# Kernel tuning notes

Hardware: AMD Instinct MI355X
Metric: run time of the kernel (lower is better)

The kernel has to match this reference:

```python
import jax, jax.numpy as jnp
import numpy as np

B, SQ, SKV, D = 4, 4096, 4096, 64

def setup_inputs() -> dict:
    key = jax.random.key(0)
    kq, kv = jax.random.split(key)
    query = jax.random.normal(kq, (B, SQ, D), dtype=jnp.float32)
    value = jax.random.normal(kv, (B, SKV, D), dtype=jnp.float32)
    return {"query": query, "value": value}

def reference(query, value):
    # scores = Q @ V^T  (value acts as both keys and values; no 1/sqrt(d) scaling)
    scores = jnp.einsum('bqd,bkd->bqk', query, value)  # [B, SQ, SKV]
    dist = jax.nn.softmax(scores, axis=-1)
    context = jnp.einsum('bqk,bkd->bqd', dist, value)  # [B, SQ, D]
    return context
```

## Files before the change

### kernel.cpp

```cpp
#include <hip/hip_runtime.h>
#include <type_traits>


#define NB   4
#define SQ   4096
#define SKV  4096
#define DH   64
#define L2E  1.44269504088896340736f

typedef _Float16 half8 __attribute__((ext_vector_type(8)));
typedef _Float16 half4 __attribute__((ext_vector_type(4)));
typedef _Float16 half2v __attribute__((ext_vector_type(2)));
typedef float f32x4 __attribute__((ext_vector_type(4)));
typedef unsigned short u16;

#define MFMA16(a, b, c) __builtin_amdgcn_mfma_f32_16x16x16f16((a), (b), (c), 0, 0, 0)
#define MFMA32(a, b, c) __builtin_amdgcn_mfma_f32_16x16x32_f16((a), (b), (c), 0, 0, 0)

__device__ __forceinline__ u16 f2h(float f) {
  _Float16 h = (_Float16)f;
  return __builtin_bit_cast(u16, h);
}
__device__ __forceinline__ half2v pkrtz(float a, float b) {
  return __builtin_bit_cast(half2v, __builtin_amdgcn_cvt_pkrtz(a, b));
}
__device__ __forceinline__ float fmax3(float a, float b, float c) {
  return fmaxf(fmaxf(a, b), c);
}

typedef __attribute__((address_space(1))) void gvoid;
typedef __attribute__((address_space(3))) void lvoid;
__device__ __forceinline__ void dma16(const u16* g, u16* l) {
  __builtin_amdgcn_global_load_lds((gvoid*)g, (lvoid*)l, 16, 0, 0);
}

__global__ __launch_bounds__(256) void prep_kernel(
    const float* __restrict__ V, u16* __restrict__ vh, u16* __restrict__ vt) {
  __shared__ u16 ldsT[16 * 72];
  int blk = blockIdx.x;
  int x   = blk & 7;
  int b   = x >> 1;
  int rem = ((x & 1) << 7) + (blk >> 3);
  int j0  = (rem >> 2) << 6;
  int d0  = (rem & 3) << 4;
  int t   = threadIdx.x;
  int j   = t >> 2;
  int dc  = (t & 3) << 2;

  const float* src = V + ((size_t)(b * SKV) + j0 + j) * DH + d0 + dc;
  float4 v4 = *(const float4*)src;
  u16 h[4] = {f2h(v4.x), f2h(v4.y), f2h(v4.z), f2h(v4.w)};
  unsigned p0 = (unsigned)h[0] | ((unsigned)h[1] << 16);
  unsigned p1 = (unsigned)h[2] | ((unsigned)h[3] << 16);
  int dfull = d0 + dc;
  int physd = ((((dfull >> 3) ^ (j & 7)) << 3)) + (dfull & 7);
  *(uint2*)(vh + ((size_t)(b * SKV) + j0 + j) * DH + physd) = make_uint2(p0, p1);

#pragma unroll
  for (int k = 0; k < 4; ++k) ldsT[(dc + k) * 72 + j] = h[k];
  __syncthreads();

  int dl = t >> 4;
  int jc = (t & 15) << 2;
  u16 tr[4];
#pragma unroll
  for (int k = 0; k < 4; ++k) tr[k] = ldsT[dl * 72 + jc + k];
  unsigned q0 = (unsigned)tr[0] | ((unsigned)tr[1] << 16);
  unsigned q1 = (unsigned)tr[2] | ((unsigned)tr[3] << 16);
  int d   = d0 + dl;
  int kc2 = jc >> 5;
  int g   = (jc >> 4) & 1;
  int qd  = (jc >> 2) & 3;
  int hp  = ((kc2 << 2) | qd) ^ (d & 7);
  *(uint2*)(vt + ((size_t)(b * DH) + d) * SKV + j0 + (hp << 3) + (g << 2)) =
      make_uint2(q0, q1);
}

__global__ __launch_bounds__(256, 4) void attn_kernel(
    const float* __restrict__ Q,
    const u16* __restrict__ vh,
    const u16* __restrict__ vt,
    u16* __restrict__ po,
    float* __restrict__ pm,
    float* __restrict__ pl,
    int S, int kvLen) {
  __shared__ __align__(16) u16 lds[2][2][4096];

  int blk  = blockIdx.x;
  int tile, s;
  if (S == 4) {
    int x  = blk & 7;
    int jj = ((x & 1) << 7) + (blk >> 3);
    tile   = ((x >> 1) << 6) + (jj >> 2);
    s      = jj & 3;
  } else {
    tile = blk / S;
    s    = blk - tile * S;
  }
  int b    = tile >> 6;
  int q0   = (tile & 63) << 6;
  int kv0  = s * kvLen;
  int t    = threadIdx.x;
  int wave = t >> 6;
  int lane = t & 63;
  int col  = lane & 15;
  int quad = lane >> 4;
  int qw   = q0 + (wave << 4);
  int c7   = col & 7;

  const u16* gv  = vh + (size_t)(b * SKV) * DH;
  const u16* gvt = vt + (size_t)(b * DH) * SKV;

  int r0 = t >> 3;
  int c0 = (t & 7) << 3;
  int wb = wave << 9;

  half8 qf[2];
#pragma unroll
  for (int kc = 0; kc < 2; ++kc) {
    const float* qp = Q + ((size_t)(b * SQ) + qw + col) * DH + kc * 32 + (quad << 3);
    float4 a0 = *(const float4*)qp;
    float4 a1 = *(const float4*)(qp + 4);
    half8 hq;
    hq[0] = (_Float16)(a0.x * L2E); hq[1] = (_Float16)(a0.y * L2E);
    hq[2] = (_Float16)(a0.z * L2E); hq[3] = (_Float16)(a0.w * L2E);
    hq[4] = (_Float16)(a1.x * L2E); hq[5] = (_Float16)(a1.y * L2E);
    hq[6] = (_Float16)(a1.z * L2E); hq[7] = (_Float16)(a1.w * L2E);
    qf[kc] = hq;
  }

  f32x4 o[4];
#pragma unroll
  for (int nf = 0; nf < 4; ++nf) o[nf] = (f32x4){0.f, 0.f, 0.f, 0.f};
  float m_r = -1e30f, l_r = 0.f;

  half4 pf[4];
  half8 vr[8];

  int ch0 = quad ^ c7;
  int ch1 = ch0 ^ 4;
  const char* Lb = (const char*)&lds[0][0][0];
  const char* a0p = Lb + (col << 7) + (ch0 << 4);
  const char* a1p = Lb + (col << 7) + (ch1 << 4);

  const u16* pvh  = gv + ((size_t)(kv0 + r0) << 6) + c0;
  const u16* pvh2 = pvh + 2048;
  const u16* pvt  = gvt + (size_t)r0 * SKV + kv0 + c0;
  const u16* pvt2 = pvt + (size_t)32 * SKV;

  dma16(pvh,  &lds[0][0][0] + wb);
  dma16(pvh2, &lds[0][0][0] + 2048 + wb);
  dma16(pvt,  &lds[0][1][0] + wb);
  dma16(pvt2, &lds[0][1][0] + 2048 + wb);
  pvh += 4096; pvh2 += 4096; pvt += 64; pvt2 += 64;

  int nIter = kvLen >> 6;

  auto body = [&](auto BUFC, int it_) {
    constexpr int BUF = decltype(BUFC)::value;
    constexpr int BO  = BUF * 16384;
    __syncthreads();

    if (it_ + 1 < nIter) {
      dma16(pvh,  &lds[BUF ^ 1][0][0] + wb);
      dma16(pvh2, &lds[BUF ^ 1][0][0] + 2048 + wb);
      dma16(pvt,  &lds[BUF ^ 1][1][0] + wb);
      dma16(pvt2, &lds[BUF ^ 1][1][0] + 2048 + wb);
    }
    pvh += 4096; pvh2 += 4096; pvt += 64; pvt2 += 64;

    __builtin_amdgcn_s_setprio(1);
    if (it_ > 0) {
#pragma unroll
      for (int kc2 = 0; kc2 < 2; ++kc2) {
#pragma unroll
        for (int nf2 = 0; nf2 < 4; ++nf2) {
          half8 w8 = vr[kc2 * 4 + nf2];
          half4 wlo = __builtin_shufflevector(w8, w8, 0, 1, 2, 3);
          half4 whi = __builtin_shufflevector(w8, w8, 4, 5, 6, 7);
          o[nf2] = MFMA16(wlo, pf[kc2 * 2], o[nf2]);
          o[nf2] = MFMA16(whi, pf[kc2 * 2 + 1], o[nf2]);
        }
      }
    }

    f32x4 sf[4];
#pragma unroll
    for (int nf = 0; nf < 4; ++nf) sf[nf] = (f32x4){0.f, 0.f, 0.f, 0.f};
#pragma unroll
    for (int nf = 0; nf < 4; ++nf) {
      half8 av0 = *(const half8*)(a0p + BO + nf * 2048);
      sf[nf] = MFMA32(av0, qf[0], sf[nf]);
      half8 av1 = *(const half8*)(a1p + BO + nf * 2048);
      sf[nf] = MFMA32(av1, qf[1], sf[nf]);
    }
    __builtin_amdgcn_s_setprio(0);

    {
      float t0 = fmax3(sf[0][0], sf[0][1], sf[0][2]);
      float t1 = fmax3(sf[0][3], sf[1][0], sf[1][1]);
      float t2 = fmax3(sf[1][2], sf[1][3], sf[2][0]);
      float t3 = fmax3(sf[2][1], sf[2][2], sf[2][3]);
      float t4 = fmax3(sf[3][0], sf[3][1], sf[3][2]);
      float t5 = fmax3(t0, t1, sf[3][3]);
      float tm = fmax3(t2, t3, t4);
      tm = fmaxf(tm, t5);
      tm = fmaxf(tm, __shfl_xor(tm, 16, 64));
      tm = fmaxf(tm, __shfl_xor(tm, 32, 64));
      float mn = fmaxf(m_r, tm);
      float al = 1.0f;
      if (!__all(mn == m_r)) {
        al = exp2f(m_r - mn);
        m_r = mn;
#pragma unroll
        for (int nf = 0; nf < 4; ++nf)
#pragma unroll
          for (int r = 0; r < 4; ++r) o[nf][r] *= al;
      }
      float rs = 0.f;
#pragma unroll
      for (int nf = 0; nf < 4; ++nf) {
        float p0 = exp2f(sf[nf][0] - mn);
        float p1 = exp2f(sf[nf][1] - mn);
        float p2 = exp2f(sf[nf][2] - mn);
        float p3 = exp2f(sf[nf][3] - mn);
        rs += (p0 + p1) + (p2 + p3);
        half2v lo = pkrtz(p0, p1);
        half2v hi = pkrtz(p2, p3);
        pf[nf] = __builtin_shufflevector(lo, hi, 0, 1, 2, 3);
      }
      l_r = l_r * al + rs;
    }

#pragma unroll
    for (int nf2 = 0; nf2 < 4; ++nf2) {
      vr[nf2]     = *(const half8*)(a0p + BO + 8192 + nf2 * 2048);
      vr[4 + nf2] = *(const half8*)(a1p + BO + 8192 + nf2 * 2048);
    }
  };

  for (int it = 0; it < nIter; it += 2) {
    body(std::integral_constant<int, 0>{}, it);
    body(std::integral_constant<int, 1>{}, it + 1);
  }

  __builtin_amdgcn_s_setprio(1);
#pragma unroll
  for (int kc2 = 0; kc2 < 2; ++kc2) {
#pragma unroll
    for (int nf2 = 0; nf2 < 4; ++nf2) {
      half8 w8 = vr[kc2 * 4 + nf2];
      half4 wlo = __builtin_shufflevector(w8, w8, 0, 1, 2, 3);
      half4 whi = __builtin_shufflevector(w8, w8, 4, 5, 6, 7);
      o[nf2] = MFMA16(wlo, pf[kc2 * 2], o[nf2]);
      o[nf2] = MFMA16(whi, pf[kc2 * 2 + 1], o[nf2]);
    }
  }
  __builtin_amdgcn_s_setprio(0);

  l_r += __shfl_xor(l_r, 16, 64);
  l_r += __shfl_xor(l_r, 32, 64);
  int pidx = tile * S + s;
  if (quad == 0) {
    pm[(size_t)pidx * 64 + (wave << 4) + col] = m_r;
    pl[(size_t)pidx * 64 + (wave << 4) + col] = l_r;
  }

  __syncthreads();
  u16* tp = &lds[0][0][0];
  {
    int qrow = (wave << 4) + col;
#pragma unroll
    for (int nf2 = 0; nf2 < 4; ++nf2) {
#pragma unroll
      for (int r2 = 0; r2 < 4; r2 += 2) {
        unsigned pk = (unsigned)f2h(o[nf2][r2]) |
                      ((unsigned)f2h(o[nf2][r2 + 1]) << 16);
        int d = nf2 * 16 + (quad << 2) + r2;
        *(unsigned*)(tp + qrow * 72 + d) = pk;
      }
    }
  }
  __syncthreads();
  {
    u16* pob = po + (size_t)pidx * 64 * 64;
    int q = t >> 2, hc = (t & 3) << 4;
    uint4 x0 = *(const uint4*)(tp + q * 72 + hc);
    uint4 x1 = *(const uint4*)(tp + q * 72 + hc + 8);
    *(uint4*)(pob + q * 64 + hc)     = x0;
    *(uint4*)(pob + q * 64 + hc + 8) = x1;
  }
}

__global__ __launch_bounds__(256) void combine_kernel(
    const u16* __restrict__ po,
    const float* __restrict__ pm,
    const float* __restrict__ pl,
    float* __restrict__ out, int S) {
  int t    = threadIdx.x;
  int rowg;
  if (S == 4) {
    int x  = blockIdx.x & 7;
    int j2 = ((x & 1) << 6) + (blockIdx.x >> 3);
    int tile = ((x >> 1) << 6) + (j2 >> 1);
    rowg = tile * 64 + ((j2 & 1) << 5) + (t >> 3);
  } else {
    rowg = blockIdx.x * 32 + (t >> 3);
  }
  int tile = rowg >> 6;
  int row  = rowg & 63;
  int dc   = (t & 7) << 3;

  float mv[8], lv[8];
  float M = -1e30f;
#pragma unroll
  for (int s = 0; s < 8; ++s) {
    if (s < S) {
      mv[s] = pm[(size_t)(tile * S + s) * 64 + row];
      lv[s] = pl[(size_t)(tile * S + s) * 64 + row];
      M = fmaxf(M, mv[s]);
    }
  }
  float L = 0.f, w[8];
#pragma unroll
  for (int s = 0; s < 8; ++s) {
    if (s < S) {
      w[s] = exp2f(mv[s] - M);
      L += lv[s] * w[s];
    }
  }
  float acc[8] = {0.f, 0.f, 0.f, 0.f, 0.f, 0.f, 0.f, 0.f};
#pragma unroll
  for (int s = 0; s < 8; ++s) {
    if (s < S) {
      const u16* p = po + (size_t)(tile * S + s) * 4096 + row * 64 + dc;
      uint4 raw = *(const uint4*)p;
      half8 x = __builtin_bit_cast(half8, raw);
#pragma unroll
      for (int k = 0; k < 8; ++k) acc[k] += w[s] * (float)x[k];
    }
  }
  float invL = 1.0f / L;
  float* op = out + (size_t)rowg * 64 + dc;
  f32x4 o0 = (f32x4){acc[0], acc[1], acc[2], acc[3]};
  f32x4 o1 = (f32x4){acc[4], acc[5], acc[6], acc[7]};
  *(f32x4*)op       = o0 * invL;
  *(f32x4*)(op + 4) = o1 * invL;
}

extern "C" void kernel_launch(void* const* d_in, const int* in_sizes, int n_in,
                              void* d_out, int out_size, void* d_ws, size_t ws_size,
                              hipStream_t stream) {
  const float* Q = (const float*)d_in[0];
  const float* V = (const float*)d_in[1];
  float* out = (float*)d_out;

  const size_t convBytes = (size_t)2 * NB * SKV * DH * 2;
  auto partBytes = [](int S) {
    return (size_t)NB * 64 * S * ((size_t)64 * 64 * 2 + 64 * 8);
  };
  int S = 4;
  while (S > 1 && ws_size < convBytes + partBytes(S)) S >>= 1;
  int kvLen = SKV / S;

  u16* vh = (u16*)d_ws;
  u16* vt = vh + (size_t)NB * SKV * DH;
  u16* po = vt + (size_t)NB * SKV * DH;
  float* pm = (float*)(po + (size_t)NB * 64 * S * 64 * 64);
  float* pl = pm + (size_t)NB * 64 * S * 64;

  prep_kernel<<<NB * 256, 256, 0, stream>>>(V, vh, vt);
  attn_kernel<<<NB * 64 * S, 256, 0, stream>>>(Q, vh, vt, po, pm, pl, S, kvLen);
  combine_kernel<<<NB * SQ / 32, 256, 0, stream>>>(po, pm, pl, out, S);
}
```

Measured before the change: 105.5 us.

## Interleave deferred PV MFMAs with QK row-max cross-lane shuffles

Moves the deferred P·V MFMAs from the previous iteration so they run after the QK score MFMAs. Each half is placed between the two cross-lane shuffle steps of the row-max reduction, so shuffle latency overlaps with matrix work. The accumulator rescale by alpha is moved after the exp/pack loop. This lengthens live ranges of the sf/pf/vr registers and could raise register pressure or change how the scheduler orders work.

```diff
diff --git a/kernel.cpp b/kernel.cpp
--- a/kernel.cpp
+++ b/kernel.cpp
@@ -169,24 +169,10 @@
     }
     pvh += 4096; pvh2 += 4096; pvt += 64; pvt2 += 64;
 
+    f32x4 sf[4];
+#pragma unroll
+    for (int nf = 0; nf < 4; ++nf) sf[nf] = (f32x4){0.f, 0.f, 0.f, 0.f};
     __builtin_amdgcn_s_setprio(1);
-    if (it_ > 0) {
-#pragma unroll
-      for (int kc2 = 0; kc2 < 2; ++kc2) {
-#pragma unroll
-        for (int nf2 = 0; nf2 < 4; ++nf2) {
-          half8 w8 = vr[kc2 * 4 + nf2];
-          half4 wlo = __builtin_shufflevector(w8, w8, 0, 1, 2, 3);
-          half4 whi = __builtin_shufflevector(w8, w8, 4, 5, 6, 7);
-          o[nf2] = MFMA16(wlo, pf[kc2 * 2], o[nf2]);
-          o[nf2] = MFMA16(whi, pf[kc2 * 2 + 1], o[nf2]);
-        }
-      }
-    }
-
-    f32x4 sf[4];
-#pragma unroll
-    for (int nf = 0; nf < 4; ++nf) sf[nf] = (f32x4){0.f, 0.f, 0.f, 0.f};
 #pragma unroll
     for (int nf = 0; nf < 4; ++nf) {
       half8 av0 = *(const half8*)(a0p + BO + nf * 2048);
@@ -196,26 +182,53 @@
     }
     __builtin_amdgcn_s_setprio(0);
 
+    float t0 = fmax3(sf[0][0], sf[0][1], sf[0][2]);
+    float t1 = fmax3(sf[0][3], sf[1][0], sf[1][1]);
+    float t2 = fmax3(sf[1][2], sf[1][3], sf[2][0]);
+    float t3 = fmax3(sf[2][1], sf[2][2], sf[2][3]);
+    float t4 = fmax3(sf[3][0], sf[3][1], sf[3][2]);
+    float t5 = fmax3(t0, t1, sf[3][3]);
+    float tmw = fmax3(t2, t3, t4);
+    tmw = fmaxf(tmw, t5);
+    float tx = __shfl_xor(tmw, 16, 64);
+
+    if (it_ > 0) {
+      __builtin_amdgcn_s_setprio(1);
+#pragma unroll
+      for (int nf2 = 0; nf2 < 4; ++nf2) {
+        half8 w8 = vr[nf2];
+        half4 wlo = __builtin_shufflevector(w8, w8, 0, 1, 2, 3);
+        half4 whi = __builtin_shufflevector(w8, w8, 4, 5, 6, 7);
+        o[nf2] = MFMA16(wlo, pf[0], o[nf2]);
+        o[nf2] = MFMA16(whi, pf[1], o[nf2]);
+      }
+      __builtin_amdgcn_s_setprio(0);
+    }
+
+    float tm2 = fmaxf(tmw, tx);
+    float ty = __shfl_xor(tm2, 32, 64);
+
+    if (it_ > 0) {
+      __builtin_amdgcn_s_setprio(1);
+#pragma unroll
+      for (int nf2 = 0; nf2 < 4; ++nf2) {
+        half8 w8 = vr[4 + nf2];
+        half4 wlo = __builtin_shufflevector(w8, w8, 0, 1, 2, 3);
+        half4 whi = __builtin_shufflevector(w8, w8, 4, 5, 6, 7);
+        o[nf2] = MFMA16(wlo, pf[2], o[nf2]);
+        o[nf2] = MFMA16(whi, pf[3], o[nf2]);
+      }
+      __builtin_amdgcn_s_setprio(0);
+    }
+
     {
-      float t0 = fmax3(sf[0][0], sf[0][1], sf[0][2]);
-      float t1 = fmax3(sf[0][3], sf[1][0], sf[1][1]);
-      float t2 = fmax3(sf[1][2], sf[1][3], sf[2][0]);
-      float t3 = fmax3(sf[2][1], sf[2][2], sf[2][3]);
-      float t4 = fmax3(sf[3][0], sf[3][1], sf[3][2]);
-      float t5 = fmax3(t0, t1, sf[3][3]);
-      float tm = fmax3(t2, t3, t4);
-      tm = fmaxf(tm, t5);
-      tm = fmaxf(tm, __shfl_xor(tm, 16, 64));
-      tm = fmaxf(tm, __shfl_xor(tm, 32, 64));
+      float tm = fmaxf(tm2, ty);
       float mn = fmaxf(m_r, tm);
       float al = 1.0f;
-      if (!__all(mn == m_r)) {
+      bool need = !__all(mn == m_r);
+      if (need) {
         al = exp2f(m_r - mn);
         m_r = mn;
-#pragma unroll
-        for (int nf = 0; nf < 4; ++nf)
-#pragma unroll
-          for (int r = 0; r < 4; ++r) o[nf][r] *= al;
       }
       float rs = 0.f;
 #pragma unroll
@@ -228,6 +241,12 @@
         half2v lo = pkrtz(p0, p1);
         half2v hi = pkrtz(p2, p3);
         pf[nf] = __builtin_shufflevector(lo, hi, 0, 1, 2, 3);
+      }
+      if (need) {
+#pragma unroll
+        for (int nf = 0; nf < 4; ++nf)
+#pragma unroll
+          for (int r = 0; r < 4; ++r) o[nf][r] *= al;
       }
       l_r = l_r * al + rs;
     }
```

Result: no change. 105.4 us (-0.1%).

## Software-pipeline softmax exponentials one iteration behind the QK MFMA

Applied to the files above, without the earlier changes.

Scores now go into alternating sfA and sfB register buffers. The exp2, P packing and output rescale for the previous tile run at the start of the next iteration, before that iteration's QK and PV MFMAs are issued. The aim is to let the transcendental and VALU work of the softmax overlap with the matrix-core work instead of serializing after the QK MFMA in the same iteration. In exchange it keeps an extra set of score registers live and adds an epilogue that drains the final tile.

```diff
diff --git a/kernel.cpp b/kernel.cpp
--- a/kernel.cpp
+++ b/kernel.cpp
@@ -136,6 +136,11 @@
 
   half4 pf[4];
   half8 vr[8];
+  f32x4 sfA[4], sfB[4];
+#pragma unroll
+  for (int nf = 0; nf < 4; ++nf) { sfA[nf] = (f32x4){0,0,0,0}; sfB[nf] = (f32x4){0,0,0,0}; }
+  float al_s = 1.0f;
+  bool  need_s = false;
 
   int ch0 = quad ^ c7;
   int ch1 = ch0 ^ 4;
@@ -156,7 +161,7 @@
 
   int nIter = kvLen >> 6;
 
-  auto body = [&](auto BUFC, int it_) {
+  auto body = [&](auto BUFC, f32x4 (&sf)[4], f32x4 (&sfo)[4], int it_) {
     constexpr int BUF = decltype(BUFC)::value;
     constexpr int BO  = BUF * 16384;
     __syncthreads();
@@ -169,7 +174,38 @@
     }
     pvh += 4096; pvh2 += 4096; pvt += 64; pvt2 += 64;
 
+    float rs = 0.f;
+    if (it_ > 0) {
+#pragma unroll
+      for (int nf = 0; nf < 4; ++nf) {
+        float p0 = exp2f(sfo[nf][0] - m_r);
+        float p1 = exp2f(sfo[nf][1] - m_r);
+        float p2 = exp2f(sfo[nf][2] - m_r);
+        float p3 = exp2f(sfo[nf][3] - m_r);
+        rs += (p0 + p1) + (p2 + p3);
+        half2v lo = pkrtz(p0, p1);
+        half2v hi = pkrtz(p2, p3);
+        pf[nf] = __builtin_shufflevector(lo, hi, 0, 1, 2, 3);
+      }
+      if (need_s) {
+#pragma unroll
+        for (int nf = 0; nf < 4; ++nf)
+#pragma unroll
+          for (int r = 0; r < 4; ++r) o[nf][r] *= al_s;
+      }
+      l_r = l_r * al_s + rs;
+    }
+
+#pragma unroll
+    for (int nf = 0; nf < 4; ++nf) sf[nf] = (f32x4){0.f, 0.f, 0.f, 0.f};
     __builtin_amdgcn_s_setprio(1);
+#pragma unroll
+    for (int nf = 0; nf < 4; ++nf) {
+      half8 av0 = *(const half8*)(a0p + BO + nf * 2048);
+      sf[nf] = MFMA32(av0, qf[0], sf[nf]);
+      half8 av1 = *(const half8*)(a1p + BO + nf * 2048);
+      sf[nf] = MFMA32(av1, qf[1], sf[nf]);
+    }
     if (it_ > 0) {
 #pragma unroll
       for (int kc2 = 0; kc2 < 2; ++kc2) {
@@ -183,17 +219,6 @@
         }
       }
     }
-
-    f32x4 sf[4];
-#pragma unroll
-    for (int nf = 0; nf < 4; ++nf) sf[nf] = (f32x4){0.f, 0.f, 0.f, 0.f};
-#pragma unroll
-    for (int nf = 0; nf < 4; ++nf) {
-      half8 av0 = *(const half8*)(a0p + BO + nf * 2048);
-      sf[nf] = MFMA32(av0, qf[0], sf[nf]);
-      half8 av1 = *(const half8*)(a1p + BO + nf * 2048);
-      sf[nf] = MFMA32(av1, qf[1], sf[nf]);
-    }
     __builtin_amdgcn_s_setprio(0);
 
     {
@@ -203,33 +228,17 @@
       float t3 = fmax3(sf[2][1], sf[2][2], sf[2][3]);
       float t4 = fmax3(sf[3][0], sf[3][1], sf[3][2]);
       float t5 = fmax3(t0, t1, sf[3][3]);
-      float tm = fmax3(t2, t3, t4);
-      tm = fmaxf(tm, t5);
-      tm = fmaxf(tm, __shfl_xor(tm, 16, 64));
-      tm = fmaxf(tm, __shfl_xor(tm, 32, 64));
-      float mn = fmaxf(m_r, tm);
-      float al = 1.0f;
-      if (!__all(mn == m_r)) {
-        al = exp2f(m_r - mn);
+      float tmw = fmax3(t2, t3, t4);
+      tmw = fmaxf(tmw, t5);
+      tmw = fmaxf(tmw, __shfl_xor(tmw, 16, 64));
+      tmw = fmaxf(tmw, __shfl_xor(tmw, 32, 64));
+      float mn = fmaxf(m_r, tmw);
+      need_s = !__all(mn == m_r);
+      al_s = 1.0f;
+      if (need_s) {
+        al_s = exp2f(m_r - mn);
         m_r = mn;
-#pragma unroll
-        for (int nf = 0; nf < 4; ++nf)
-#pragma unroll
-          for (int r = 0; r < 4; ++r) o[nf][r] *= al;
-      }
-      float rs = 0.f;
-#pragma unroll
-      for (int nf = 0; nf < 4; ++nf) {
-        float p0 = exp2f(sf[nf][0] - mn);
-        float p1 = exp2f(sf[nf][1] - mn);
-        float p2 = exp2f(sf[nf][2] - mn);
-        float p3 = exp2f(sf[nf][3] - mn);
-        rs += (p0 + p1) + (p2 + p3);
-        half2v lo = pkrtz(p0, p1);
-        half2v hi = pkrtz(p2, p3);
-        pf[nf] = __builtin_shufflevector(lo, hi, 0, 1, 2, 3);
-      }
-      l_r = l_r * al + rs;
+      }
     }
 
 #pragma unroll
@@ -240,23 +249,44 @@
   };
 
   for (int it = 0; it < nIter; it += 2) {
-    body(std::integral_constant<int, 0>{}, it);
-    body(std::integral_constant<int, 1>{}, it + 1);
-  }
-
-  __builtin_amdgcn_s_setprio(1);
-#pragma unroll
-  for (int kc2 = 0; kc2 < 2; ++kc2) {
-#pragma unroll
-    for (int nf2 = 0; nf2 < 4; ++nf2) {
-      half8 w8 = vr[kc2 * 4 + nf2];
-      half4 wlo = __builtin_shufflevector(w8, w8, 0, 1, 2, 3);
-      half4 whi = __builtin_shufflevector(w8, w8, 4, 5, 6, 7);
-      o[nf2] = MFMA16(wlo, pf[kc2 * 2], o[nf2]);
-      o[nf2] = MFMA16(whi, pf[kc2 * 2 + 1], o[nf2]);
-    }
-  }
-  __builtin_amdgcn_s_setprio(0);
+    body(std::integral_constant<int, 0>{}, sfA, sfB, it);
+    body(std::integral_constant<int, 1>{}, sfB, sfA, it + 1);
+  }
+
+  {
+    float rs = 0.f;
+#pragma unroll
+    for (int nf = 0; nf < 4; ++nf) {
+      float p0 = exp2f(sfB[nf][0] - m_r);
+      float p1 = exp2f(sfB[nf][1] - m_r);
+      float p2 = exp2f(sfB[nf][2] - m_r);
+      float p3 = exp2f(sfB[nf][3] - m_r);
+      rs += (p0 + p1) + (p2 + p3);
+      half2v lo = pkrtz(p0, p1);
+      half2v hi = pkrtz(p2, p3);
+      pf[nf] = __builtin_shufflevector(lo, hi, 0, 1, 2, 3);
+    }
+    if (need_s) {
+#pragma unroll
+      for (int nf = 0; nf < 4; ++nf)
+#pragma unroll
+        for (int r = 0; r < 4; ++r) o[nf][r] *= al_s;
+    }
+    l_r = l_r * al_s + rs;
+    __builtin_amdgcn_s_setprio(1);
+#pragma unroll
+    for (int kc2 = 0; kc2 < 2; ++kc2) {
+#pragma unroll
+      for (int nf2 = 0; nf2 < 4; ++nf2) {
+        half8 w8 = vr[kc2 * 4 + nf2];
+        half4 wlo = __builtin_shufflevector(w8, w8, 0, 1, 2, 3);
+        half4 whi = __builtin_shufflevector(w8, w8, 4, 5, 6, 7);
+        o[nf2] = MFMA16(wlo, pf[kc2 * 2], o[nf2]);
+        o[nf2] = MFMA16(whi, pf[kc2 * 2 + 1], o[nf2]);
+      }
+    }
+    __builtin_amdgcn_s_setprio(0);
+  }
 
   l_r += __shfl_xor(l_r, 16, 64);
   l_r += __shfl_xor(l_r, 32, 64);
```

Result: no change. 105.9 us (+0.4%).
